# Performance work log

Measured on AMD Instinct MI355X. Metric: run time of the kernel, lower is better.

## Reference

```python
import jax, jax.numpy as jnp
import numpy as np

B, NVIS, NHID, NCLASS = 2048, 2048, 1024, 64


def setup_inputs() -> dict:
    key = jax.random.key(0)
    k1, k2, k3, k4, k5 = jax.random.split(key, 5)
    return {
        "v": jax.random.normal(k1, (B, NVIS), dtype=jnp.float32),
        "W": jax.random.normal(k2, (NVIS, NHID), dtype=jnp.float32),
        "c": jax.random.normal(k3, (1, NHID), dtype=jnp.float32),
        "d": jax.random.normal(k4, (1, NCLASS), dtype=jnp.float32),
        "U": jax.random.normal(k5, (NCLASS, NHID), dtype=jnp.float32),
    }


def reference(v, W, c, d, U):
    # precomputed_factor: [B, nhid]
    pre = jnp.matmul(v, W) + c
    # class free energies F[b, y] = d[0, y] + sum_j softplus(pre[b, j] + U[y, j])
    # broadcast to [B, nclass, nhid], reduce over hidden units
    F = d[0] + jnp.sum(jax.nn.softplus(pre[:, None, :] + U[None, :, :]), axis=-1)  # [B, nclass]
    # pairwise normalization 1 / sum_d exp(F_d - F_c) == softmax(F) along classes
    class_probs = jax.nn.softmax(F, axis=1)
    max_idx = jnp.argmax(class_probs, axis=1)
    one_hot = jax.nn.one_hot(max_idx, U.shape[0], dtype=jnp.int32)
    return class_probs, one_hot
```

## Files before the change

### kernel.cpp

```cpp
#include <hip/hip_runtime.h>

constexpr int kB    = 2048;
constexpr int kVIS  = 2048;
constexpr int kHID  = 1024;
constexpr int kCLS  = 64;
constexpr float kLog2e = 1.4426950408889634f;

typedef __attribute__((ext_vector_type(8))) short bf16x8;
typedef __attribute__((ext_vector_type(4))) float f32x4;
typedef __attribute__((ext_vector_type(2))) float f32x2;

typedef __attribute__((address_space(3))) unsigned       as3_u32;
typedef __attribute__((address_space(1))) const unsigned as1_u32;

__device__ __forceinline__ void g2lds16(const void* g, void* l) {
    __builtin_amdgcn_global_load_lds((as1_u32*)g, (as3_u32*)l, 16, 0, 0);
}

__device__ __forceinline__ unsigned short f2bf(float x) {
    unsigned u = __float_as_uint(x);
    u += 0x7fffu + ((u >> 16) & 1u);
    return (unsigned short)(u >> 16);
}
__device__ __forceinline__ float bf2f(unsigned short h) {
    return __uint_as_float(((unsigned)h) << 16);
}

__global__ __launch_bounds__(256) void prep_all(const float* __restrict__ v,
                                                const float* __restrict__ W,
                                                const float* __restrict__ U,
                                                unsigned short* __restrict__ vh,
                                                unsigned short* __restrict__ vl,
                                                unsigned short* __restrict__ wth,
                                                unsigned short* __restrict__ wtl,
                                                float* __restrict__ Utp) {
    __shared__ float T[64][65];
    const int bx = blockIdx.x;
    if (bx < 4096) {
        const int i = (bx * 256 + threadIdx.x) * 4;
        const float4 xv = *(const float4*)(v + i);
        ushort4 h, l;
        h.x = f2bf(xv.x); l.x = f2bf(xv.x - bf2f(h.x));
        h.y = f2bf(xv.y); l.y = f2bf(xv.y - bf2f(h.y));
        h.z = f2bf(xv.z); l.z = f2bf(xv.z - bf2f(h.z));
        h.w = f2bf(xv.w); l.w = f2bf(xv.w - bf2f(h.w));
        *(ushort4*)(vh + i) = h;
        *(ushort4*)(vl + i) = l;
    } else if (bx < 4608) {
        const int b = bx - 4096;
        const int n0 = (b & 15) * 64;
        const int k0 = (b >> 4) * 64;
        const int c = threadIdx.x & 63, r0 = threadIdx.x >> 6;
#pragma unroll
        for (int ps = 0; ps < 16; ++ps) {
            const int r = r0 + ps * 4;
            T[r][c] = W[(size_t)(k0 + r) * kHID + n0 + c];
        }
        __syncthreads();
#pragma unroll
        for (int ps = 0; ps < 16; ++ps) {
            const int nn = r0 + ps * 4;
            const float x = T[c][nn];
            const unsigned short h = f2bf(x);
            const unsigned short l = f2bf(x - bf2f(h));
            const size_t o = (size_t)(n0 + nn) * kVIS + k0 + c;
            wth[o] = h;
            wtl[o] = l;
        }
    } else {
        const int id = (bx - 4608) * 256 + threadIdx.x;
        const int j = id >> 6, y = id & 63;
        Utp[(((j >> 2) * kCLS + y) << 2) + (j & 3)] = U[(size_t)y * kHID + j] * kLog2e;
    }
}

__global__ __launch_bounds__(1024, 1) void gemm_fused(const unsigned short* __restrict__ vh,
                                                      const unsigned short* __restrict__ vl,
                                                      const unsigned short* __restrict__ wth,
                                                      const unsigned short* __restrict__ wtl,
                                                      const float* __restrict__ cvec,
                                                      const float* __restrict__ Utp,
                                                      float* __restrict__ Fpart) {
    constexpr int kSlabElems = 24576;
    __shared__ __align__(16) union SMem {
        unsigned short stage[3][kSlabElems];
        float psH[2][128][68];
    } smem;

    const int tid = threadIdx.x;
    const int lane = tid & 63, wave = tid >> 6;
    const int mh = wave >> 2;
    const int nh = (wave >> 1) & 1;
    const int kh = wave & 1;

    const int bid = blockIdx.x;
    const int x = bid & 7, s = bid >> 3;
    const int ncol = (x << 1) | (s & 1);
    const int mstripe = s >> 1;
    const int m0 = mstripe << 7, n0 = ncol << 6;

    const int rA = tid >> 3, qA = tid & 7;
    const int octA = (qA ^ (rA & 7)) << 3;
    const unsigned short* const srcAh = vh + (size_t)(m0 + rA) * kVIS + octA;
    const unsigned short* const srcAl = vl + (size_t)(m0 + rA) * kVIS + octA;
    const int tb = tid & 511;
    const int rB = tb >> 3, qB = tb & 7;
    const int octB = (qB ^ (rB & 7)) << 3;
    const unsigned short* const srcB =
        ((tid < 512) ? wth : wtl) + (size_t)(n0 + rB) * kVIS + octB;
    const int dOff = tid << 3;

    unsigned short* const st = &smem.stage[0][0];

    const int fm = lane & 15, fq = lane >> 4;
    const int p = (((kh << 2) + fq) ^ (fm & 7)) << 3;
    const int ar0 = ((mh * 32 + fm) << 6) + p;
    const int ar1 = ar0 + (16 << 6);
    const int br0 = 16384 + ((nh * 32 + fm) << 6) + p;
    const int br1 = br0 + (16 << 6);

    f32x4 acc[2][2] = {};

    auto stage_slab = [&](int slab, unsigned short* buf) {
        const int koff = slab << 6;
        g2lds16(srcAh + koff, buf + dOff);
        g2lds16(srcAl + koff, buf + 8192 + dOff);
        g2lds16(srcB + koff, buf + 16384 + dOff);
    };
    auto compute = [&](const unsigned short* buf) {
        const bf16x8 a_h0 = *(const bf16x8*)(buf + ar0);
        const bf16x8 a_h1 = *(const bf16x8*)(buf + ar1);
        const bf16x8 a_l0 = *(const bf16x8*)(buf + 8192 + ar0);
        const bf16x8 a_l1 = *(const bf16x8*)(buf + 8192 + ar1);
        const bf16x8 b_h0 = *(const bf16x8*)(buf + br0);
        const bf16x8 b_h1 = *(const bf16x8*)(buf + br1);
        const bf16x8 b_l0 = *(const bf16x8*)(buf + 4096 + br0);
        const bf16x8 b_l1 = *(const bf16x8*)(buf + 4096 + br1);
        acc[0][0] = __builtin_amdgcn_mfma_f32_16x16x32_bf16(a_h0, b_h0, acc[0][0], 0, 0, 0);
        acc[0][0] = __builtin_amdgcn_mfma_f32_16x16x32_bf16(a_h0, b_l0, acc[0][0], 0, 0, 0);
        acc[0][0] = __builtin_amdgcn_mfma_f32_16x16x32_bf16(a_l0, b_h0, acc[0][0], 0, 0, 0);
        acc[0][1] = __builtin_amdgcn_mfma_f32_16x16x32_bf16(a_h0, b_h1, acc[0][1], 0, 0, 0);
        acc[0][1] = __builtin_amdgcn_mfma_f32_16x16x32_bf16(a_h0, b_l1, acc[0][1], 0, 0, 0);
        acc[0][1] = __builtin_amdgcn_mfma_f32_16x16x32_bf16(a_l0, b_h1, acc[0][1], 0, 0, 0);
        acc[1][0] = __builtin_amdgcn_mfma_f32_16x16x32_bf16(a_h1, b_h0, acc[1][0], 0, 0, 0);
        acc[1][0] = __builtin_amdgcn_mfma_f32_16x16x32_bf16(a_h1, b_l0, acc[1][0], 0, 0, 0);
        acc[1][0] = __builtin_amdgcn_mfma_f32_16x16x32_bf16(a_l1, b_h0, acc[1][0], 0, 0, 0);
        acc[1][1] = __builtin_amdgcn_mfma_f32_16x16x32_bf16(a_h1, b_h1, acc[1][1], 0, 0, 0);
        acc[1][1] = __builtin_amdgcn_mfma_f32_16x16x32_bf16(a_h1, b_l1, acc[1][1], 0, 0, 0);
        acc[1][1] = __builtin_amdgcn_mfma_f32_16x16x32_bf16(a_l1, b_h1, acc[1][1], 0, 0, 0);
    };

    stage_slab(0, st);
    stage_slab(1, st + kSlabElems);

    unsigned short* bufPrev = st + 2 * kSlabElems;
    unsigned short* bufCur  = st;
    unsigned short* bufNext = st + kSlabElems;

    for (int t = 0; t < 31; ++t) {
        asm volatile("s_waitcnt vmcnt(3)" ::: "memory");
        __builtin_amdgcn_s_barrier();
        __builtin_amdgcn_sched_barrier(0);
        compute(bufCur);
        __builtin_amdgcn_s_barrier();
        __builtin_amdgcn_sched_barrier(0);
        if (t < 30) stage_slab(t + 2, bufPrev);
        unsigned short* tmp = bufPrev; bufPrev = bufCur; bufCur = bufNext; bufNext = tmp;
    }
    asm volatile("s_waitcnt vmcnt(0)" ::: "memory");
    __builtin_amdgcn_s_barrier();
    __builtin_amdgcn_sched_barrier(0);
    compute(bufCur);
    __syncthreads();

#pragma unroll
    for (int j = 0; j < 2; ++j) {
        const int col = nh * 32 + j * 16 + fm;
        const float cadd = kh ? 0.f : cvec[n0 + col];
#pragma unroll
        for (int i = 0; i < 2; ++i) {
            const int rbase = mh * 32 + i * 16 + fq * 4;
#pragma unroll
            for (int rr = 0; rr < 4; ++rr)
                smem.psH[kh][rbase + rr][col] = (acc[i][j][rr] + cadd) * kLog2e;
        }
    }
    __syncthreads();

#pragma unroll
    for (int s2 = 0; s2 < 2; ++s2) {
        const int id = tid + (s2 << 10);
        const int row = id >> 4, q = id & 15;
        float4* d = (float4*)&smem.psH[0][row][q << 2];
        const float4* a = (const float4*)&smem.psH[1][row][q << 2];
        const float4 va = *a, vd = *d;
        *d = make_float4(vd.x + va.x, vd.y + va.y, vd.z + va.z, vd.w + va.w);
    }
    __syncthreads();

    const int q0 = (n0 >> 2);
    f32x2 relu2[8], prod2[8];
#pragma unroll
    for (int rr = 0; rr < 8; ++rr) { relu2[rr] = (f32x2)(0.f); prod2[rr] = (f32x2)(1.f); }

    const f32x2 zero2 = (f32x2)(0.f);
    for (int jc = 0; jc < 64; jc += 8) {
        const float4 ua = ((const float4*)Utp)[(q0 + (jc >> 2) + 0) * kCLS + lane];
        const float4 ub = ((const float4*)Utp)[(q0 + (jc >> 2) + 1) * kCLS + lane];
        const f32x2 u01 = {ua.x, ua.y}, u23 = {ua.z, ua.w};
        const f32x2 u45 = {ub.x, ub.y}, u67 = {ub.z, ub.w};
#pragma unroll
        for (int rr = 0; rr < 8; ++rr) {
            const int row = wave * 8 + rr;
            const float4 p0 = *(const float4*)&smem.psH[0][row][jc];
            const float4 p1 = *(const float4*)&smem.psH[0][row][jc + 4];
            f32x2 tp[4];
            tp[0] = (f32x2){p0.x, p0.y} + u01;
            tp[1] = (f32x2){p0.z, p0.w} + u23;
            tp[2] = (f32x2){p1.x, p1.y} + u45;
            tp[3] = (f32x2){p1.z, p1.w} + u67;
#pragma unroll
            for (int g = 0; g < 4; ++g) {
                const f32x2 t = tp[g];
                f32x2 e;
                e.x = __builtin_amdgcn_exp2f(-__builtin_fabsf(t.x));
                e.y = __builtin_amdgcn_exp2f(-__builtin_fabsf(t.y));
                prod2[rr] = __builtin_elementwise_fma(prod2[rr], e, prod2[rr]);
                relu2[rr] += __builtin_elementwise_max(t, zero2);
            }
        }
    }
#pragma unroll
    for (int rr = 0; rr < 8; ++rr) {
        const float contrib = relu2[rr].x + relu2[rr].y +
                              __builtin_amdgcn_logf(prod2[rr].x * prod2[rr].y);
        Fpart[((size_t)ncol * kB + m0 + wave * 8 + rr) * kCLS + lane] = contrib;
    }
}

__global__ __launch_bounds__(256) void softmax_final(const float* __restrict__ Fpart,
                                                     const float* __restrict__ dvec,
                                                     float* __restrict__ out) {
    const int tid = threadIdx.x;
    const int lane = tid & 63, wave = tid >> 6;
    const int row = blockIdx.x * 4 + wave;
    double s = 0.0;
#pragma unroll
    for (int k = 0; k < kHID / 64; ++k)
        s += (double)Fpart[((size_t)k * kB + row) * kCLS + lane];
    const float G = (float)s + dvec[lane] * kLog2e;

    float m = G;
    int mi = lane;
#pragma unroll
    for (int off = 32; off; off >>= 1) {
        const float om = __shfl_xor(m, off);
        const int   oi = __shfl_xor(mi, off);
        if (om > m || (om == m && oi < mi)) { m = om; mi = oi; }
    }
    const float e2 = __builtin_amdgcn_exp2f(G - m);
    float ssum = e2;
#pragma unroll
    for (int off = 32; off; off >>= 1) ssum += __shfl_xor(ssum, off);
    out[(size_t)row * kCLS + lane] = e2 / ssum;
    out[(size_t)kB * kCLS + (size_t)row * kCLS + lane] = (lane == mi) ? 1.0f : 0.0f;
}

constexpr int BM = 64, BN = 64, BK = 16;

__global__ __launch_bounds__(256) void gemm_vw(const float* __restrict__ V,
                                               const float* __restrict__ Wm,
                                               const float* __restrict__ cvec,
                                               float* __restrict__ pre) {
    __shared__ float As[BK][BM + 4];
    __shared__ float Bs[BK][BN + 4];
    const int tid = threadIdx.x;
    const int tx = tid & 15, ty = tid >> 4;
    const int m0 = blockIdx.y * BM, n0 = blockIdx.x * BN;
    const int arow = tid >> 2, acol = (tid & 3) << 2;
    const int brow = tid >> 4, bcol = (tid & 15) << 2;
    const float* vptr = V + (size_t)(m0 + arow) * kVIS + acol;
    const float* wptr = Wm + (size_t)brow * kHID + n0 + bcol;
    float acc[4][4] = {};
    for (int k0 = 0; k0 < kVIS; k0 += BK) {
        const float4 a4 = *(const float4*)(vptr + k0);
        const float4 b4 = *(const float4*)(wptr + (size_t)k0 * kHID);
        __syncthreads();
        As[acol + 0][arow] = a4.x; As[acol + 1][arow] = a4.y;
        As[acol + 2][arow] = a4.z; As[acol + 3][arow] = a4.w;
        *(float4*)&Bs[brow][bcol] = b4;
        __syncthreads();
#pragma unroll
        for (int k = 0; k < BK; ++k) {
            const float4 av = *(const float4*)&As[k][ty << 2];
            const float4 bv = *(const float4*)&Bs[k][tx << 2];
            const float a[4] = {av.x, av.y, av.z, av.w};
            const float b[4] = {bv.x, bv.y, bv.z, bv.w};
#pragma unroll
            for (int i = 0; i < 4; ++i)
#pragma unroll
                for (int j = 0; j < 4; ++j) acc[i][j] += a[i] * b[j];
        }
    }
#pragma unroll
    for (int i = 0; i < 4; ++i) {
        const int row = m0 + (ty << 2) + i;
        const int col = n0 + (tx << 2);
        const float4 cv = *(const float4*)(cvec + col);
        float4 o;
        o.x = acc[i][0] + cv.x; o.y = acc[i][1] + cv.y;
        o.z = acc[i][2] + cv.z; o.w = acc[i][3] + cv.w;
        *(float4*)(pre + (size_t)row * kHID + col) = o;
    }
}

__device__ __forceinline__ float softplus_f(float x) {
    return fmaxf(x, 0.f) + __logf(1.f + __expf(-fabsf(x)));
}

__global__ __launch_bounds__(256) void classify(const float* __restrict__ pre,
                                                const float* __restrict__ U,
                                                const float* __restrict__ dvec,
                                                float* __restrict__ out) {
    __shared__ float preS[4][kHID];
    __shared__ float Fs[4][kCLS];
    const int tid = threadIdx.x;
    const int lane = tid & 63, wave = tid >> 6;
    const int b0 = blockIdx.x * 4;
    const float4* src = (const float4*)(pre + (size_t)b0 * kHID);
    float4* dst = (float4*)preS;
    for (int i = tid; i < kHID; i += 256) dst[i] = src[i];
    __syncthreads();
    for (int yi = 0; yi < 16; ++yi) {
        const int y = (wave << 4) + yi;
        const float* Uy = U + (size_t)y * kHID;
        float a0 = 0.f, a1 = 0.f, a2 = 0.f, a3 = 0.f;
#pragma unroll
        for (int it = 0; it < kHID / 64; ++it) {
            const int j = lane + (it << 6);
            const float u = Uy[j];
            a0 += softplus_f(preS[0][j] + u);
            a1 += softplus_f(preS[1][j] + u);
            a2 += softplus_f(preS[2][j] + u);
            a3 += softplus_f(preS[3][j] + u);
        }
        double d0 = a0, d1 = a1, d2 = a2, d3 = a3;
#pragma unroll
        for (int off = 32; off; off >>= 1) {
            d0 += __shfl_xor(d0, off); d1 += __shfl_xor(d1, off);
            d2 += __shfl_xor(d2, off); d3 += __shfl_xor(d3, off);
        }
        if (lane == 0) {
            const float dy = dvec[y];
            Fs[0][y] = (float)d0 + dy; Fs[1][y] = (float)d1 + dy;
            Fs[2][y] = (float)d2 + dy; Fs[3][y] = (float)d3 + dy;
        }
    }
    __syncthreads();
    const float F = Fs[wave][lane];
    float m = F; int mi = lane;
#pragma unroll
    for (int off = 32; off; off >>= 1) {
        const float om = __shfl_xor(m, off);
        const int oi = __shfl_xor(mi, off);
        if (om > m || (om == m && oi < mi)) { m = om; mi = oi; }
    }
    const float e = __expf(F - m);
    float s = e;
#pragma unroll
    for (int off = 32; off; off >>= 1) s += __shfl_xor(s, off);
    const int row = b0 + wave;
    out[(size_t)row * kCLS + lane] = e / s;
    out[(size_t)kB * kCLS + (size_t)row * kCLS + lane] = (lane == mi) ? 1.0f : 0.0f;
}

extern "C" void kernel_launch(void* const* d_in, const int* in_sizes, int n_in,
                              void* d_out, int out_size, void* d_ws, size_t ws_size,
                              hipStream_t stream) {
    const float* v = (const float*)d_in[0];
    const float* W = (const float*)d_in[1];
    const float* c = (const float*)d_in[2];
    const float* d = (const float*)d_in[3];
    const float* U = (const float*)d_in[4];
    float* out = (float*)d_out;
    char* ws = (char*)d_ws;

    const size_t need = 33816576;
    if (ws_size >= need) {
        unsigned short* vh  = (unsigned short*)(ws);
        unsigned short* vl  = (unsigned short*)(ws + 8388608);
        unsigned short* wth = (unsigned short*)(ws + 16777216);
        unsigned short* wtl = (unsigned short*)(ws + 20971520);
        float* Utp   = (float*)(ws + 25165824);
        float* Fpart = (float*)(ws + 25427968);
        prep_all<<<4864, 256, 0, stream>>>(v, W, U, vh, vl, wth, wtl, Utp);
        gemm_fused<<<256, 1024, 0, stream>>>(vh, vl, wth, wtl, c, Utp, Fpart);
        softmax_final<<<kB / 4, 256, 0, stream>>>(Fpart, d, out);
    } else {
        float* pre = (float*)ws;
        gemm_vw<<<dim3(kHID / BN, kB / BM), 256, 0, stream>>>(v, W, c, pre);
        classify<<<kB / 4, 256, 0, stream>>>(pre, U, d, out);
    }
}
```

Measured before the change: 130.2 us.

## Fuse fp32-to-bf16 hi/lo split of v into the GEMM main loop

Drops the separate prep pass that split v into bf16 high and low halves and wrote both to workspace. The GEMM now loads fp32 v rows into registers one slab ahead, converts them in-kernel and writes the swizzled hi/lo tiles straight to LDS. This removes a full read-and-write pass over v and a large block of the prep launch. The cost is that A staging moves from asynchronous global-to-LDS copies to register loads plus VALU conversion inside the pipelined loop, with one barrier removed and the wait changed to lgkmcnt.

```diff
diff --git a/kernel.cpp b/kernel.cpp
--- a/kernel.cpp
+++ b/kernel.cpp
@@ -26,28 +26,15 @@
     return __uint_as_float(((unsigned)h) << 16);
 }
 
-__global__ __launch_bounds__(256) void prep_all(const float* __restrict__ v,
-                                                const float* __restrict__ W,
+__global__ __launch_bounds__(256) void prep_all(const float* __restrict__ W,
                                                 const float* __restrict__ U,
-                                                unsigned short* __restrict__ vh,
-                                                unsigned short* __restrict__ vl,
                                                 unsigned short* __restrict__ wth,
                                                 unsigned short* __restrict__ wtl,
                                                 float* __restrict__ Utp) {
     __shared__ float T[64][65];
     const int bx = blockIdx.x;
-    if (bx < 4096) {
-        const int i = (bx * 256 + threadIdx.x) * 4;
-        const float4 xv = *(const float4*)(v + i);
-        ushort4 h, l;
-        h.x = f2bf(xv.x); l.x = f2bf(xv.x - bf2f(h.x));
-        h.y = f2bf(xv.y); l.y = f2bf(xv.y - bf2f(h.y));
-        h.z = f2bf(xv.z); l.z = f2bf(xv.z - bf2f(h.z));
-        h.w = f2bf(xv.w); l.w = f2bf(xv.w - bf2f(h.w));
-        *(ushort4*)(vh + i) = h;
-        *(ushort4*)(vl + i) = l;
-    } else if (bx < 4608) {
-        const int b = bx - 4096;
+    if (bx < 512) {
+        const int b = bx;
         const int n0 = (b & 15) * 64;
         const int k0 = (b >> 4) * 64;
         const int c = threadIdx.x & 63, r0 = threadIdx.x >> 6;
@@ -68,14 +55,13 @@
             wtl[o] = l;
         }
     } else {
-        const int id = (bx - 4608) * 256 + threadIdx.x;
+        const int id = (bx - 512) * 256 + threadIdx.x;
         const int j = id >> 6, y = id & 63;
         Utp[(((j >> 2) * kCLS + y) << 2) + (j & 3)] = U[(size_t)y * kHID + j] * kLog2e;
     }
 }
 
-__global__ __launch_bounds__(1024, 1) void gemm_fused(const unsigned short* __restrict__ vh,
-                                                      const unsigned short* __restrict__ vl,
+__global__ __launch_bounds__(1024, 1) void gemm_fused(const float* __restrict__ v,
                                                       const unsigned short* __restrict__ wth,
                                                       const unsigned short* __restrict__ wtl,
                                                       const float* __restrict__ cvec,
@@ -100,9 +86,10 @@
     const int m0 = mstripe << 7, n0 = ncol << 6;
 
     const int rA = tid >> 3, qA = tid & 7;
-    const int octA = (qA ^ (rA & 7)) << 3;
-    const unsigned short* const srcAh = vh + (size_t)(m0 + rA) * kVIS + octA;
-    const unsigned short* const srcAl = vl + (size_t)(m0 + rA) * kVIS + octA;
+    const int posA = qA ^ (rA & 7);
+    const float* const srcV = v + (size_t)(m0 + rA) * kVIS + (qA << 3);
+    const int dstA = (rA << 6) + (posA << 3);
+
     const int tb = tid & 511;
     const int rB = tb >> 3, qB = tb & 7;
     const int octB = (qB ^ (rB & 7)) << 3;
@@ -121,11 +108,25 @@
 
     f32x4 acc[2][2] = {};
 
-    auto stage_slab = [&](int slab, unsigned short* buf) {
-        const int koff = slab << 6;
-        g2lds16(srcAh + koff, buf + dOff);
-        g2lds16(srcAl + koff, buf + 8192 + dOff);
-        g2lds16(srcB + koff, buf + 16384 + dOff);
+    auto stage_B = [&](int slab, unsigned short* buf) {
+        g2lds16(srcB + (slab << 6), buf + 16384 + dOff);
+    };
+    auto cvt_write = [&](const f32x4& lo, const f32x4& hi, unsigned short* buf) {
+        const float xs[8] = {lo.x, lo.y, lo.z, lo.w, hi.x, hi.y, hi.z, hi.w};
+        unsigned hw[8], lw[8];
+#pragma unroll
+        for (int i = 0; i < 8; ++i) {
+            const unsigned short h = f2bf(xs[i]);
+            hw[i] = h;
+            lw[i] = f2bf(xs[i] - bf2f(h));
+        }
+        uint4 hv, lv;
+        hv.x = hw[0] | (hw[1] << 16); hv.y = hw[2] | (hw[3] << 16);
+        hv.z = hw[4] | (hw[5] << 16); hv.w = hw[6] | (hw[7] << 16);
+        lv.x = lw[0] | (lw[1] << 16); lv.y = lw[2] | (lw[3] << 16);
+        lv.z = lw[4] | (lw[5] << 16); lv.w = lw[6] | (lw[7] << 16);
+        *(uint4*)(buf + dstA) = hv;
+        *(uint4*)(buf + 8192 + dstA) = lv;
     };
     auto compute = [&](const unsigned short* buf) {
         const bf16x8 a_h0 = *(const bf16x8*)(buf + ar0);
@@ -150,24 +151,37 @@
         acc[1][1] = __builtin_amdgcn_mfma_f32_16x16x32_bf16(a_l1, b_h1, acc[1][1], 0, 0, 0);
     };
 
-    stage_slab(0, st);
-    stage_slab(1, st + kSlabElems);
+    stage_B(0, st);
+    stage_B(1, st + kSlabElems);
+    f32x4 aC0 = *(const f32x4*)(srcV);
+    f32x4 aC1 = *(const f32x4*)(srcV + 4);
+    f32x4 aN0 = *(const f32x4*)(srcV + 64);
+    f32x4 aN1 = *(const f32x4*)(srcV + 68);
+    cvt_write(aC0, aC1, st);
+    aC0 = aN0; aC1 = aN1;
 
     unsigned short* bufPrev = st + 2 * kSlabElems;
     unsigned short* bufCur  = st;
     unsigned short* bufNext = st + kSlabElems;
 
     for (int t = 0; t < 31; ++t) {
-        asm volatile("s_waitcnt vmcnt(3)" ::: "memory");
+        asm volatile("s_waitcnt lgkmcnt(0)" ::: "memory");
         __builtin_amdgcn_s_barrier();
         __builtin_amdgcn_sched_barrier(0);
         compute(bufCur);
-        __builtin_amdgcn_s_barrier();
+        if (t < 30) {
+            stage_B(t + 2, bufPrev);
+            __builtin_amdgcn_sched_barrier(0);
+            const int ko = (t + 2) << 6;
+            aN0 = *(const f32x4*)(srcV + ko);
+            aN1 = *(const f32x4*)(srcV + ko + 4);
+        }
         __builtin_amdgcn_sched_barrier(0);
-        if (t < 30) stage_slab(t + 2, bufPrev);
+        cvt_write(aC0, aC1, bufNext);
+        aC0 = aN0; aC1 = aN1;
         unsigned short* tmp = bufPrev; bufPrev = bufCur; bufCur = bufNext; bufNext = tmp;
     }
-    asm volatile("s_waitcnt vmcnt(0)" ::: "memory");
+    asm volatile("s_waitcnt lgkmcnt(0)" ::: "memory");
     __builtin_amdgcn_s_barrier();
     __builtin_amdgcn_sched_barrier(0);
     compute(bufCur);
@@ -387,14 +401,12 @@
 
     const size_t need = 33816576;
     if (ws_size >= need) {
-        unsigned short* vh  = (unsigned short*)(ws);
-        unsigned short* vl  = (unsigned short*)(ws + 8388608);
         unsigned short* wth = (unsigned short*)(ws + 16777216);
         unsigned short* wtl = (unsigned short*)(ws + 20971520);
         float* Utp   = (float*)(ws + 25165824);
         float* Fpart = (float*)(ws + 25427968);
-        prep_all<<<4864, 256, 0, stream>>>(v, W, U, vh, vl, wth, wtl, Utp);
-        gemm_fused<<<256, 1024, 0, stream>>>(vh, vl, wth, wtl, c, Utp, Fpart);
+        prep_all<<<768, 256, 0, stream>>>(W, U, wth, wtl, Utp);
+        gemm_fused<<<256, 1024, 0, stream>>>(v, wth, wtl, c, Utp, Fpart);
         softmax_final<<<kB / 4, 256, 0, stream>>>(Fpart, d, out);
     } else {
         float* pre = (float*)ws;
```

New measurement: 137.1 us. 1.05x slower.
